# Optimization experiments

Measured on AMD Instinct MI355X. Metric: run time of the kernel, lower is better.

Reference implementation:

```python
import jax, jax.numpy as jnp
import numpy as np

NUM_NODES = 200000
NUM_EDGES = 500000
B = 4096            # batch size (src, dst, neg each B)
ND = 3 * B          # dst nodes of attention block
K = 10              # sampled neighbors per dst
N = ND * (1 + K)    # total tail nodes
D = 128             # dim_embed == dim_node
DE = 128            # dim_edge
DT = 128            # dim_time
H = 2               # num_heads
DIN = 2 * D + DE + DT  # GRUCell input dim


def time_encode(t, w, b):
    # tglite TimeEncode: cos(t * w + b)
    return jnp.cos(t[..., None] * w + b)


def gru_cell(x, h, w_ih, w_hh, b_ih, b_hh):
    # torch.nn.GRUCell, gate order [r, z, n]
    gi = x @ w_ih.T + b_ih
    gh = h @ w_hh.T + b_hh
    i_r, i_z, i_n = jnp.split(gi, 3, axis=-1)
    h_r, h_z, h_n = jnp.split(gh, 3, axis=-1)
    r = jax.nn.sigmoid(i_r + h_r)
    z = jax.nn.sigmoid(i_z + h_z)
    n = jnp.tanh(i_n + r * h_n)
    return (1.0 - z) * n + z * h


def setup_inputs() -> dict:
    key = jax.random.key(0)
    ks = jax.random.split(key, 40)
    p = lambda i, shape: jax.random.normal(ks[i], shape, dtype=jnp.float32) * 0.05
    return {
        "nodes": jax.random.randint(ks[0], (N,), 0, NUM_NODES),
        "eids": jax.random.randint(ks[1], (ND, K), 0, NUM_EDGES),
        "dt_nbr": jax.random.uniform(ks[2], (ND, K), dtype=jnp.float32) * 1000.0,
        "nfeat": p(3, (NUM_NODES, D)),
        "mem_data": p(4, (NUM_NODES, D)),
        "mem_time": jax.random.uniform(ks[5], (NUM_NODES,), dtype=jnp.float32) * 1000.0,
        "mail_data": p(6, (NUM_NODES, 2 * D + DE)),
        "mail_time": jax.random.uniform(ks[7], (NUM_NODES,), dtype=jnp.float32) * 1000.0,
        "efeat": p(8, (NUM_EDGES, DE)),
        "time_w": p(9, (DT,)),
        "time_b": p(10, (DT,)),
        "gru_w_ih": p(11, (3 * D, DIN)),
        "gru_w_hh": p(12, (3 * D, D)),
        "gru_b_ih": p(13, (3 * D,)),
        "gru_b_hh": p(14, (3 * D,)),
        "wq": p(15, (D, D + DT)), "bq": p(16, (D,)),
        "wk": p(17, (D, D + DE + DT)), "bk": p(18, (D,)),
        "wv": p(19, (D, D + DE + DT)), "bv": p(20, (D,)),
        "wo": p(21, (D, 2 * D)), "bo": p(22, (D,)),
        "ln_g": jnp.ones((D,), jnp.float32), "ln_b": jnp.zeros((D,), jnp.float32),
        "ep_sw": p(23, (D, D)), "ep_sb": p(24, (D,)),
        "ep_dw": p(25, (D, D)), "ep_db": p(26, (D,)),
        "ep_ow": p(27, (1, D)), "ep_ob": p(28, (1,)),
    }


def reference(nodes, eids, dt_nbr, nfeat, mem_data, mem_time, mail_data, mail_time,
              efeat, time_w, time_b, gru_w_ih, gru_w_hh, gru_b_ih, gru_b_hh,
              wq, bq, wk, bk, wv, bv, wo, bo, ln_g, ln_b,
              ep_sw, ep_sb, ep_dw, ep_db, ep_ow, ep_ob):
    # ---- update_memory: gather mailbox/memory, time-encode delta, GRUCell ----
    delta = mail_time[nodes] - mem_time[nodes]                  # [N]
    tenc = time_encode(delta, time_w, time_b)                   # [N, DT]
    mail = jnp.concatenate([mail_data[nodes], tenc], axis=1)    # [N, DIN]
    mem = gru_cell(mail, mem_data[nodes], gru_w_ih, gru_w_hh, gru_b_ih, gru_b_hh)  # [N, D]
    # (blk.g.mem.update(nodes, mem, mail_ts) is a persistent-state side effect)

    h = nfeat[nodes] + mem                                      # dst/src hidden states
    dst_h = h[:ND]                                              # [ND, D]
    src_h = h[ND:].reshape(ND, K, D)                            # [ND, K, D]

    # ---- TemporalAttnLayer (TGL-style multi-head attention over neighbors) ----
    zero_tenc = jnp.broadcast_to(jnp.cos(time_b), (ND, DT))     # time_encode(0)
    Q = jnp.concatenate([dst_h, zero_tenc], axis=1) @ wq.T + bq # [ND, D]
    tenc_n = time_encode(dt_nbr, time_w, time_b)                # [ND, K, DT]
    k_in = jnp.concatenate([src_h, efeat[eids], tenc_n], axis=-1)  # [ND, K, D+DE+DT]
    Kf = k_in @ wk.T + bk                                       # [ND, K, D]
    Vf = k_in @ wv.T + bv                                       # [ND, K, D]

    dh = D // H
    Qh = Q.reshape(ND, H, dh)
    Kh = Kf.reshape(ND, K, H, dh)
    Vh = Vf.reshape(ND, K, H, dh)
    att = jax.nn.softmax(jnp.einsum('nhd,nkhd->nkh', Qh, Kh), axis=1)  # [ND, K, H]
    agg = jnp.einsum('nkh,nkhd->nhd', att, Vh).reshape(ND, D)   # [ND, D]

    out = jnp.concatenate([dst_h, agg], axis=1) @ wo.T + bo     # [ND, D]
    out = jax.nn.relu(out)
    mu = out.mean(axis=-1, keepdims=True)
    var = out.var(axis=-1, keepdims=True)
    emb = ln_g * (out - mu) * jax.lax.rsqrt(var + 1e-5) + ln_b  # LayerNorm

    # ---- EdgePredictor over (src, dst) and (src, neg) splits ----
    src_e, dst_e, neg_e = emb[:B], emb[B:2 * B], emb[2 * B:]
    s_proj = src_e @ ep_sw.T + ep_sb
    pos = jax.nn.relu(s_proj + dst_e @ ep_dw.T + ep_db) @ ep_ow.T + ep_ob  # [B, 1]
    neg = jax.nn.relu(s_proj + neg_e @ ep_dw.T + ep_db) @ ep_ow.T + ep_ob  # [B, 1]
    return jnp.concatenate([pos, neg], axis=1)                  # [B, 2]
```

## Files before the change

### kernel.cpp

```cpp
#include <hip/hip_runtime.h>

constexpr int ND_   = 12288;
constexpr int K_    = 10;
constexpr int NTOT  = ND_ * (1 + K_);
constexpr int B_    = 4096;
constexpr int RKV   = ND_ * K_;

constexpr size_t OFF_QB   = 0;
constexpr size_t OFF_AGG  = 786432;
constexpr size_t OFF_HB   = 43253760;
constexpr size_t OFF_KVB  = 51904512;
constexpr size_t OFF_EMB  = 67633152;
constexpr size_t OFF_WCAT = 69206016;
constexpr size_t OFF_WKV  = 69369856;
constexpr size_t OFF_BCAT = 69419008;
constexpr size_t OFF_BKV  = 69419520;
constexpr size_t OFF_WQB  = 69419776;
constexpr size_t OFF_WOB  = 69427968;
constexpr size_t OFF_SWP  = 69444352;
constexpr size_t OFF_DWP  = 69460736;
constexpr size_t OFF_QZ   = 69477120;

#define DEVFN __device__ __forceinline__

typedef __attribute__((ext_vector_type(8))) short bf16x8;
typedef __attribute__((ext_vector_type(4))) float f32x4;
#define MFMA16(a, b, c) __builtin_amdgcn_mfma_f32_16x16x32_bf16((a), (b), (c), 0, 0, 0)

DEVFN unsigned short f2bf(float x) {
  unsigned int u = __float_as_uint(x);
  u = (u + 0x7FFFu + ((u >> 16) & 1u)) >> 16;
  return (unsigned short)u;
}
DEVFN float bf2f(unsigned short h) { return __uint_as_float(((unsigned int)h) << 16); }

DEVFN bf16x8 packcvt(float4 a, float4 b) {
  union { unsigned int u[4]; bf16x8 v; } r;
  asm("v_cvt_pk_bf16_f32 %0, %1, %2" : "=v"(r.u[0]) : "v"(a.x), "v"(a.y));
  asm("v_cvt_pk_bf16_f32 %0, %1, %2" : "=v"(r.u[1]) : "v"(a.z), "v"(a.w));
  asm("v_cvt_pk_bf16_f32 %0, %1, %2" : "=v"(r.u[2]) : "v"(b.x), "v"(b.y));
  asm("v_cvt_pk_bf16_f32 %0, %1, %2" : "=v"(r.u[3]) : "v"(b.z), "v"(b.w));
  return r.v;
}

DEVFN float dot4(const float4 a, const float4 b, float acc) {
  acc = fmaf(a.x, b.x, acc);
  acc = fmaf(a.y, b.y, acc);
  acc = fmaf(a.z, b.z, acc);
  acc = fmaf(a.w, b.w, acc);
  return acc;
}
DEVFN float fsig(float x)  { return __fdividef(1.0f, 1.0f + __expf(-x)); }
DEVFN float ftanh(float x) {
  x = fminf(fmaxf(x, -15.0f), 15.0f);
  const float t = __expf(2.0f * x);
  return __fdividef(t - 1.0f, t + 1.0f);
}

__global__ void k0_all(const float* __restrict__ w_ih, const float* __restrict__ w_hh,
                       const float* __restrict__ wk,   const float* __restrict__ wv,
                       const float* __restrict__ wq,   const float* __restrict__ wo,
                       const float* __restrict__ sw,   const float* __restrict__ dwm,
                       const float* __restrict__ b_ih, const float* __restrict__ b_hh,
                       const float* __restrict__ bk,   const float* __restrict__ bv,
                       const float* __restrict__ time_b, const float* __restrict__ bq,
                       unsigned short* __restrict__ WcatP, unsigned short* __restrict__ WkvP,
                       unsigned short* __restrict__ WqB,   unsigned short* __restrict__ WoB,
                       float4* __restrict__ SwP, float4* __restrict__ DwP,
                       float* __restrict__ bcat, float* __restrict__ bkv,
                       float* __restrict__ qzero)
{
  int gid = blockIdx.x * 256 + threadIdx.x;
  if (gid < 327680) {
    int f = gid >> 9, idx = gid & 511;
    int l = idx >> 3, j8 = idx & 7;
    int kt = f >> 5, nt = f & 31;
    int k = kt * 32 + (l >> 4) * 8 + j8;
    int c = nt * 16 + (l & 15);
    int q = c >> 7, jb = (c >> 6) & 1, g = (c >> 4) & 3, j = q * 32 + jb * 16 + (c & 15);
    float w;
    if (g == 0)      w = (k < 512) ? w_ih[(size_t)j * 512 + k]         : w_hh[(size_t)j * 128 + (k - 512)];
    else if (g == 1) w = (k < 512) ? w_ih[(size_t)(128 + j) * 512 + k] : w_hh[(size_t)(128 + j) * 128 + (k - 512)];
    else if (g == 2) w = (k < 512) ? w_ih[(size_t)(256 + j) * 512 + k] : 0.0f;
    else             w = (k < 512) ? 0.0f : w_hh[(size_t)(256 + j) * 128 + (k - 512)];
    WcatP[gid] = f2bf(w);
    return;
  }
  gid -= 327680;
  if (gid < 98304) {
    int f = gid >> 9, idx = gid & 511;
    int l = idx >> 3, j8 = idx & 7;
    int kt = f >> 4, nt = f & 15;
    int k = kt * 32 + (l >> 4) * 8 + j8;
    int c = nt * 16 + (l & 15);
    float w = (c < 128) ? wk[(size_t)c * 384 + k] : wv[(size_t)(c - 128) * 384 + k];
    WkvP[gid] = f2bf(w);
    return;
  }
  gid -= 98304;
  if (gid < 49152) {
    if (gid < 16384) {
      int f = gid >> 9, idx = gid & 511;
      int l = idx >> 3, j8 = idx & 7;
      int kt = f >> 3, nt = f & 7;
      int k = kt * 32 + (l >> 4) * 8 + j8;
      int c = nt * 16 + (l & 15);
      WqB[gid] = f2bf(wq[(size_t)c * 256 + k]);
    } else {
      int g2 = gid - 16384;
      int f = g2 >> 9, idx = g2 & 511;
      int l = idx >> 3, j8 = idx & 7;
      int kt = f >> 3, nt = f & 7;
      int k = kt * 32 + (l >> 4) * 8 + j8;
      int c = nt * 16 + (l & 15);
      WoB[g2] = f2bf(wo[(size_t)c * 256 + k]);
    }
    return;
  }
  gid -= 49152;
  if (gid < 8960) {
    if (gid < 4096) {
      int k4 = gid / 128, c = gid % 128;
      const float* s = sw + c * 128 + 4 * k4;
      SwP[gid] = make_float4(s[0], s[1], s[2], s[3]);
    } else if (gid < 8192) {
      int id = gid - 4096;
      int k4 = id / 128, c = id % 128;
      const float* s = dwm + c * 128 + 4 * k4;
      DwP[id] = make_float4(s[0], s[1], s[2], s[3]);
    } else if (gid < 8704) {
      int id = gid - 8192;
      int q = id >> 7, jb = (id >> 6) & 1, g = (id >> 4) & 3, lcc = id & 15;
      int j = q * 32 + jb * 16 + lcc;
      float b;
      if (g == 0)      b = b_ih[j] + b_hh[j];
      else if (g == 1) b = b_ih[128 + j] + b_hh[128 + j];
      else if (g == 2) b = b_ih[256 + j];
      else             b = b_hh[256 + j];
      bcat[id] = b;
    } else {
      int id = gid - 8704;
      bkv[id] = (id < 128) ? bk[id] : bv[id - 128];
    }
    return;
  }
  gid -= 8960;
  if (gid < 128) {
    float acc = bq[gid];
    for (int k = 0; k < 128; ++k)
      acc = fmaf(cosf(time_b[k]), wq[gid * 256 + 128 + k], acc);
    qzero[gid] = acc;
  }
}

__global__ __launch_bounds__(512, 4) void k1_fused(
    const int* __restrict__ nodes, const float* __restrict__ mail_data,
    const float* __restrict__ mem_data, const float* __restrict__ mail_time,
    const float* __restrict__ mem_time, const float* __restrict__ time_w,
    const float* __restrict__ time_b, const unsigned short* __restrict__ WcatP,
    const float* __restrict__ bcat, const float* __restrict__ nfeat,
    unsigned short* __restrict__ hb)
{
  __shared__ unsigned short As[20 * 1024];
  const int tid = threadIdx.x;
  const int rbase = blockIdx.x * 32;

  {
    const int sr = tid & 31, scol = tid >> 5;
    const int q = scol & 3, koff = scol >> 2;
    const int n = nodes[rbase + sr];
    const float drow = mail_time[n] - mem_time[n];
    const float* mailp = mail_data + (size_t)n * 384;
    const float* memp  = mem_data  + (size_t)n * 128;
    unsigned short* wb = As + (size_t)((sr >> 4) * 64 + q * 16 + (sr & 15)) * 8;
    #pragma unroll
    for (int i = 0; i < 5; ++i) {
      const int kt = 4 * i + koff;
      const int c0 = kt * 32 + q * 8;
      float4 v0, v1;
      if (c0 < 384) {
        v0 = *(const float4*)(mailp + c0);
        v1 = *(const float4*)(mailp + c0 + 4);
      } else if (c0 >= 512) {
        v0 = *(const float4*)(memp + c0 - 512);
        v1 = *(const float4*)(memp + c0 - 508);
      } else {
        const float4 w0 = *(const float4*)(time_w + c0 - 384);
        const float4 w1 = *(const float4*)(time_w + c0 - 380);
        const float4 b0 = *(const float4*)(time_b + c0 - 384);
        const float4 b1 = *(const float4*)(time_b + c0 - 380);
        v0.x = __cosf(fmaf(drow, w0.x, b0.x)); v0.y = __cosf(fmaf(drow, w0.y, b0.y));
        v0.z = __cosf(fmaf(drow, w0.z, b0.z)); v0.w = __cosf(fmaf(drow, w0.w, b0.w));
        v1.x = __cosf(fmaf(drow, w1.x, b1.x)); v1.y = __cosf(fmaf(drow, w1.y, b1.y));
        v1.z = __cosf(fmaf(drow, w1.z, b1.z)); v1.w = __cosf(fmaf(drow, w1.w, b1.w));
      }
      *(bf16x8*)(wb + (size_t)kt * 1024) = packcvt(v0, v1);
    }
  }
  __syncthreads();

  const int w = tid >> 6, l = tid & 63;
  const int lr = l >> 4, lc = l & 15;
  const unsigned short* Bp = WcatP + (size_t)(w * 4) * 512 + l * 8;
  const unsigned short* Ab = As + (size_t)l * 8;

  f32x4 acc[2][4];
  #pragma unroll
  for (int m = 0; m < 2; ++m)
    #pragma unroll
    for (int bn = 0; bn < 4; ++bn) acc[m][bn] = (f32x4){0.f, 0.f, 0.f, 0.f};

  #pragma unroll
  for (int kt = 0; kt < 20; ++kt) {
    const bf16x8 A0 = *(const bf16x8*)(Ab + (size_t)kt * 1024);
    const bf16x8 A1 = *(const bf16x8*)(Ab + (size_t)kt * 1024 + 512);
    #pragma unroll
    for (int bn = 0; bn < 4; ++bn) {
      const bf16x8 Bf = *(const bf16x8*)(Bp + ((size_t)kt * 32 + bn) * 512);
      acc[0][bn] = MFMA16(A0, Bf, acc[0][bn]);
      acc[1][bn] = MFMA16(A1, Bf, acc[1][bn]);
    }
  }

  const int jcol = (w >> 1) * 32 + (w & 1) * 16 + lc;
  float bg[4];
  #pragma unroll
  for (int g = 0; g < 4; ++g) bg[g] = bcat[w * 64 + g * 16 + lc];
  const int memkt = 16 + (w >> 1);
  const int qp = (w & 1) * 2 + (lc >> 3);
  const int el = lc & 7;

  #pragma unroll
  for (int mt = 0; mt < 2; ++mt) {
    #pragma unroll
    for (int rr = 0; rr < 4; ++rr) {
      const int rloc = mt * 16 + lr * 4 + rr;
      const int grow = rbase + rloc;
      const int n2   = nodes[grow];
      const float aR  = acc[mt][0][rr] + bg[0];
      const float aZ  = acc[mt][1][rr] + bg[1];
      const float aNi = acc[mt][2][rr] + bg[2];
      const float aNh = acc[mt][3][rr] + bg[3];
      const float r_  = fsig(aR);
      const float z_  = fsig(aZ);
      const float n_  = ftanh(aNi + r_ * aNh);
      const float mem = bf2f(As[(size_t)memkt * 1024 +
                                (size_t)(mt * 64 + qp * 16 + (rloc & 15)) * 8 + el]);
      const float h = nfeat[(size_t)n2 * 128 + jcol] + (1.0f - z_) * n_ + z_ * mem;
      hb[(size_t)grow * 128 + jcol] = f2bf(h);
    }
  }
}

DEVFN void k2s(const unsigned short* __restrict__ WkvP, int kt, int wn, int l,
               bf16x8 a, f32x4 (&acc)[4]) {
  #pragma unroll
  for (int bn = 0; bn < 4; ++bn) {
    const bf16x8 b = *(const bf16x8*)(WkvP + ((size_t)(kt * 16 + wn * 4 + bn) * 64 + l) * 8);
    acc[bn] = MFMA16(a, b, acc[bn]);
  }
}

__global__ __launch_bounds__(512) void k2_fused(
    const unsigned short* __restrict__ hb, const int* __restrict__ eids,
    const float* __restrict__ dt_nbr, const float* __restrict__ efeat,
    const float* __restrict__ time_w, const float* __restrict__ time_b,
    const unsigned short* __restrict__ WkvP, const float* __restrict__ bkv,
    unsigned short* __restrict__ KVb)
{
  const int w = threadIdx.x >> 6, l = threadIdx.x & 63;
  const int wm = w >> 2, wn = w & 3;
  const int lr = l >> 4, lc = l & 15;
  const int t16 = blockIdx.x * 2 + wm;
  const int rbase = t16 * 16;

  int eld = 0; float dld = 0.f;
  if (l < 16) { eld = eids[rbase + l]; dld = dt_nbr[rbase + l]; }
  const int   eid = __shfl(eld, lc);
  const float dt  = __shfl(dld, lc);

  const float* ep = efeat + (size_t)eid * 128 + lr * 8;
  bf16x8 ea[4];
  #pragma unroll
  for (int qq = 0; qq < 4; ++qq)
    ea[qq] = packcvt(((const float4*)(ep + qq * 32))[0], ((const float4*)(ep + qq * 32))[1]);
  const unsigned short* hp = hb + (size_t)(ND_ + rbase + lc) * 128 + lr * 8;
  bf16x8 hh[4];
  #pragma unroll
  for (int qq = 0; qq < 4; ++qq) hh[qq] = *(const bf16x8*)(hp + qq * 32);
  bf16x8 tt[4];
  #pragma unroll
  for (int qq = 0; qq < 4; ++qq) {
    const int c0 = qq * 32 + lr * 8;
    const float4 w0 = ((const float4*)(time_w + c0))[0];
    const float4 w1 = ((const float4*)(time_w + c0))[1];
    const float4 b0 = ((const float4*)(time_b + c0))[0];
    const float4 b1 = ((const float4*)(time_b + c0))[1];
    float4 u, v;
    u.x = __cosf(fmaf(dt, w0.x, b0.x)); u.y = __cosf(fmaf(dt, w0.y, b0.y));
    u.z = __cosf(fmaf(dt, w0.z, b0.z)); u.w = __cosf(fmaf(dt, w0.w, b0.w));
    v.x = __cosf(fmaf(dt, w1.x, b1.x)); v.y = __cosf(fmaf(dt, w1.y, b1.y));
    v.z = __cosf(fmaf(dt, w1.z, b1.z)); v.w = __cosf(fmaf(dt, w1.w, b1.w));
    tt[qq] = packcvt(u, v);
  }

  f32x4 acc[4];
  #pragma unroll
  for (int bn = 0; bn < 4; ++bn) acc[bn] = (f32x4){0.f, 0.f, 0.f, 0.f};

  #pragma unroll
  for (int qq = 0; qq < 4; ++qq) k2s(WkvP, qq, wn, l, hh[qq], acc);
  #pragma unroll
  for (int qq = 0; qq < 4; ++qq) k2s(WkvP, 4 + qq, wn, l, ea[qq], acc);
  #pragma unroll
  for (int qq = 0; qq < 4; ++qq) k2s(WkvP, 8 + qq, wn, l, tt[qq], acc);

  float bb[4];
  #pragma unroll
  for (int bn = 0; bn < 4; ++bn) bb[bn] = bkv[wn * 64 + bn * 16 + lc];

  #pragma unroll
  for (int rr = 0; rr < 4; ++rr) {
    const size_t grow = (size_t)(rbase + lr * 4 + rr);
    #pragma unroll
    for (int bn = 0; bn < 4; ++bn)
      KVb[grow * 256 + wn * 64 + bn * 16 + lc] = f2bf(acc[bn][rr] + bb[bn]);
  }
}

__global__ __launch_bounds__(512) void kQ_gemm(
    const unsigned short* __restrict__ hb, const unsigned short* __restrict__ WqB,
    const float* __restrict__ qzero, unsigned short* __restrict__ Qb)
{
  const int w = threadIdx.x >> 6, l = threadIdx.x & 63;
  const int wm = w >> 2, wn = w & 3;
  const int lr = l >> 4, lc = l & 15;
  const int t16base = blockIdx.x * 4 + wm * 2;
  const unsigned short* Ar0 = hb + (size_t)(t16base * 16 + lc) * 128 + lr * 8;
  const unsigned short* Ar1 = Ar0 + 16 * 128;

  f32x4 acc[2][2];
  #pragma unroll
  for (int m = 0; m < 2; ++m)
    #pragma unroll
    for (int bn = 0; bn < 2; ++bn) acc[m][bn] = (f32x4){0.f, 0.f, 0.f, 0.f};

  #pragma unroll
  for (int kt = 0; kt < 4; ++kt) {
    const bf16x8 a0 = *(const bf16x8*)(Ar0 + kt * 32);
    const bf16x8 a1 = *(const bf16x8*)(Ar1 + kt * 32);
    #pragma unroll
    for (int bn = 0; bn < 2; ++bn) {
      const bf16x8 b = *(const bf16x8*)(WqB + ((size_t)(kt * 8 + wn * 2 + bn) * 64 + l) * 8);
      acc[0][bn] = MFMA16(a0, b, acc[0][bn]);
      acc[1][bn] = MFMA16(a1, b, acc[1][bn]);
    }
  }

  #pragma unroll
  for (int mt = 0; mt < 2; ++mt)
    #pragma unroll
    for (int rr = 0; rr < 4; ++rr) {
      const int row = (t16base + mt) * 16 + lr * 4 + rr;
      #pragma unroll
      for (int bn = 0; bn < 2; ++bn) {
        const int col = (wn * 2 + bn) * 16 + lc;
        Qb[(size_t)row * 128 + col] = f2bf(acc[mt][bn][rr] + qzero[col]);
      }
    }
}

__global__ __launch_bounds__(256) void kAtt(
    const unsigned short* __restrict__ Qb, const unsigned short* __restrict__ KVb,
    unsigned short* __restrict__ aggb)
{
  const int w = threadIdx.x >> 6, l = threadIdx.x & 63;
  const int i = blockIdx.x * 4 + w;
  const float q0 = bf2f(Qb[(size_t)i * 128 + l]);
  const float q1 = bf2f(Qb[(size_t)i * 128 + 64 + l]);
  const unsigned short* base = KVb + (size_t)i * K_ * 256;

  float s0[K_], s1[K_], v0[K_], v1[K_];
  #pragma unroll
  for (int kk = 0; kk < K_; ++kk) {
    const unsigned short* rp = base + kk * 256;
    const float k0 = bf2f(rp[l]);
    const float k1 = bf2f(rp[64 + l]);
    v0[kk] = bf2f(rp[128 + l]);
    v1[kk] = bf2f(rp[192 + l]);
    float p0 = q0 * k0, p1 = q1 * k1;
    #pragma unroll
    for (int t = 32; t; t >>= 1) { p0 += __shfl_xor(p0, t); p1 += __shfl_xor(p1, t); }
    s0[kk] = p0; s1[kk] = p1;
  }
  float m0 = s0[0], m1 = s1[0];
  #pragma unroll
  for (int kk = 1; kk < K_; ++kk) { m0 = fmaxf(m0, s0[kk]); m1 = fmaxf(m1, s1[kk]); }
  float sum0 = 0.f, sum1 = 0.f, a0 = 0.f, a1 = 0.f;
  #pragma unroll
  for (int kk = 0; kk < K_; ++kk) {
    const float e0 = __expf(s0[kk] - m0);
    const float e1 = __expf(s1[kk] - m1);
    sum0 += e0; sum1 += e1;
    a0 += e0 * v0[kk]; a1 += e1 * v1[kk];
  }
  aggb[(size_t)i * 128 + l]      = f2bf(__fdividef(a0, sum0));
  aggb[(size_t)i * 128 + 64 + l] = f2bf(__fdividef(a1, sum1));
}

__global__ __launch_bounds__(512) void kO_ln(
    const unsigned short* __restrict__ hb, const unsigned short* __restrict__ aggb,
    const unsigned short* __restrict__ WoB, const float* __restrict__ bo,
    const float* __restrict__ ln_g, const float* __restrict__ ln_b,
    float* __restrict__ emb)
{
  __shared__ float ps[64][4], pq[64][4];
  const int w = threadIdx.x >> 6, l = threadIdx.x & 63;
  const int wm = w >> 2, wn = w & 3;
  const int lr = l >> 4, lc = l & 15;
  const int t16base = blockIdx.x * 4 + wm * 2;
  const unsigned short* Ah0 = hb   + (size_t)(t16base * 16 + lc) * 128 + lr * 8;
  const unsigned short* Ah1 = Ah0 + 16 * 128;
  const unsigned short* Ag0 = aggb + (size_t)(t16base * 16 + lc) * 128 + lr * 8;
  const unsigned short* Ag1 = Ag0 + 16 * 128;

  f32x4 acc[2][2];
  #pragma unroll
  for (int m = 0; m < 2; ++m)
    #pragma unroll
    for (int bn = 0; bn < 2; ++bn) acc[m][bn] = (f32x4){0.f, 0.f, 0.f, 0.f};

  #pragma unroll
  for (int kt = 0; kt < 8; ++kt) {
    const bf16x8 a0 = (kt < 4) ? *(const bf16x8*)(Ah0 + kt * 32)
                               : *(const bf16x8*)(Ag0 + (kt - 4) * 32);
    const bf16x8 a1 = (kt < 4) ? *(const bf16x8*)(Ah1 + kt * 32)
                               : *(const bf16x8*)(Ag1 + (kt - 4) * 32);
    #pragma unroll
    for (int bn = 0; bn < 2; ++bn) {
      const bf16x8 b = *(const bf16x8*)(WoB + ((size_t)(kt * 8 + wn * 2 + bn) * 64 + l) * 8);
      acc[0][bn] = MFMA16(a0, b, acc[0][bn]);
      acc[1][bn] = MFMA16(a1, b, acc[1][bn]);
    }
  }

  const int c0 = (wn * 2) * 16 + lc, c1 = c0 + 16;
  const float b0v = bo[c0], b1v = bo[c1];
  float xv0[2][4], xv1[2][4];
  #pragma unroll
  for (int mt = 0; mt < 2; ++mt)
    #pragma unroll
    for (int rr = 0; rr < 4; ++rr) {
      const float x0 = fmaxf(acc[mt][0][rr] + b0v, 0.f);
      const float x1 = fmaxf(acc[mt][1][rr] + b1v, 0.f);
      xv0[mt][rr] = x0; xv1[mt][rr] = x1;
      float s = x0 + x1, q = x0 * x0 + x1 * x1;
      #pragma unroll
      for (int t = 8; t; t >>= 1) { s += __shfl_xor(s, t); q += __shfl_xor(q, t); }
      const int rloc = (wm * 2 + mt) * 16 + lr * 4 + rr;
      if (lc == 0) { ps[rloc][wn] = s; pq[rloc][wn] = q; }
    }
  __syncthreads();
  const float g0 = ln_g[c0], g1 = ln_g[c1], lb0 = ln_b[c0], lb1 = ln_b[c1];
  #pragma unroll
  for (int mt = 0; mt < 2; ++mt)
    #pragma unroll
    for (int rr = 0; rr < 4; ++rr) {
      const int rloc = (wm * 2 + mt) * 16 + lr * 4 + rr;
      const int row  = blockIdx.x * 64 + rloc;
      const float sum = ps[rloc][0] + ps[rloc][1] + ps[rloc][2] + ps[rloc][3];
      const float sq  = pq[rloc][0] + pq[rloc][1] + pq[rloc][2] + pq[rloc][3];
      const float mu  = sum * (1.0f / 128.0f);
      const float var = sq * (1.0f / 128.0f) - mu * mu;
      const float rs  = rsqrtf(var + 1e-5f);
      emb[(size_t)row * 128 + c0] = g0 * (xv0[mt][rr] - mu) * rs + lb0;
      emb[(size_t)row * 128 + c1] = g1 * (xv1[mt][rr] - mu) * rs + lb1;
    }
}

__global__ __launch_bounds__(128) void k3_ep(
    const float* __restrict__ emb, const float4* __restrict__ SwP,
    const float4* __restrict__ DwP, const float* __restrict__ ep_sb,
    const float* __restrict__ ep_db, const float* __restrict__ ep_ow,
    const float* __restrict__ ep_ob, float* __restrict__ out)
{
  __shared__ float se[128], de[128], ne[128];
  __shared__ float redp[2], redn[2];
  const int c = threadIdx.x;
  const int i = blockIdx.x;
  se[c] = emb[(size_t)i * 128 + c];
  de[c] = emb[(size_t)(B_ + i) * 128 + c];
  ne[c] = emb[(size_t)(2 * B_ + i) * 128 + c];
  __syncthreads();
  float sacc = ep_sb[c], dacc = ep_db[c], nacc = ep_db[c];
  for (int k4 = 0; k4 < 32; ++k4) {
    const float4 sw = SwP[k4 * 128 + c];
    const float4 dw = DwP[k4 * 128 + c];
    sacc = dot4(((const float4*)se)[k4], sw, sacc);
    dacc = dot4(((const float4*)de)[k4], dw, dacc);
    nacc = dot4(((const float4*)ne)[k4], dw, nacc);
  }
  const float ow = ep_ow[c];
  float pp = fmaxf(sacc + dacc, 0.f) * ow;
  float pn = fmaxf(sacc + nacc, 0.f) * ow;
  for (int t = 32; t; t >>= 1) { pp += __shfl_xor(pp, t); pn += __shfl_xor(pn, t); }
  if ((c & 63) == 0) { redp[c >> 6] = pp; redn[c >> 6] = pn; }
  __syncthreads();
  if (c == 0) {
    const float ob = ep_ob[0];
    out[i * 2]     = redp[0] + redp[1] + ob;
    out[i * 2 + 1] = redn[0] + redn[1] + ob;
  }
}

extern "C" void kernel_launch(void* const* d_in, const int* in_sizes, int n_in,
                              void* d_out, int out_size, void* d_ws, size_t ws_size,
                              hipStream_t stream) {
  const int*   nodes     = (const int*)d_in[0];
  const int*   eids      = (const int*)d_in[1];
  const float* dt_nbr    = (const float*)d_in[2];
  const float* nfeat     = (const float*)d_in[3];
  const float* mem_data  = (const float*)d_in[4];
  const float* mem_time  = (const float*)d_in[5];
  const float* mail_data = (const float*)d_in[6];
  const float* mail_time = (const float*)d_in[7];
  const float* efeat     = (const float*)d_in[8];
  const float* time_w    = (const float*)d_in[9];
  const float* time_b    = (const float*)d_in[10];
  const float* gru_w_ih  = (const float*)d_in[11];
  const float* gru_w_hh  = (const float*)d_in[12];
  const float* gru_b_ih  = (const float*)d_in[13];
  const float* gru_b_hh  = (const float*)d_in[14];
  const float* wq        = (const float*)d_in[15];
  const float* bq        = (const float*)d_in[16];
  const float* wk        = (const float*)d_in[17];
  const float* bk        = (const float*)d_in[18];
  const float* wv        = (const float*)d_in[19];
  const float* bv        = (const float*)d_in[20];
  const float* wo        = (const float*)d_in[21];
  const float* bo        = (const float*)d_in[22];
  const float* ln_g      = (const float*)d_in[23];
  const float* ln_b      = (const float*)d_in[24];
  const float* ep_sw     = (const float*)d_in[25];
  const float* ep_sb     = (const float*)d_in[26];
  const float* ep_dw     = (const float*)d_in[27];
  const float* ep_db     = (const float*)d_in[28];
  const float* ep_ow     = (const float*)d_in[29];
  const float* ep_ob     = (const float*)d_in[30];
  float* out = (float*)d_out;
  float* ws  = (float*)d_ws;

  unsigned short* Qb    = (unsigned short*)(ws + OFF_QB);
  unsigned short* aggb  = (unsigned short*)(ws + OFF_AGG);
  unsigned short* hb    = (unsigned short*)(ws + OFF_HB);
  unsigned short* KVb   = (unsigned short*)(ws + OFF_KVB);
  float*          emb   = ws + OFF_EMB;
  unsigned short* WcatP = (unsigned short*)(ws + OFF_WCAT);
  unsigned short* WkvP  = (unsigned short*)(ws + OFF_WKV);
  float*          bcat  = ws + OFF_BCAT;
  float*          bkv   = ws + OFF_BKV;
  unsigned short* WqB   = (unsigned short*)(ws + OFF_WQB);
  unsigned short* WoB   = (unsigned short*)(ws + OFF_WOB);
  float4*         SwP   = (float4*)(ws + OFF_SWP);
  float4*         DwP   = (float4*)(ws + OFF_DWP);
  float*          qzero = ws + OFF_QZ;

  k0_all<<<1892, 256, 0, stream>>>(gru_w_ih, gru_w_hh, wk, wv, wq, wo, ep_sw, ep_dw,
                                   gru_b_ih, gru_b_hh, bk, bv, time_b, bq,
                                   WcatP, WkvP, WqB, WoB, SwP, DwP, bcat, bkv, qzero);
  k1_fused<<<NTOT / 32, 512, 0, stream>>>(nodes, mail_data, mem_data, mail_time,
                                          mem_time, time_w, time_b, WcatP, bcat,
                                          nfeat, hb);
  k2_fused<<<RKV / 32, 512, 0, stream>>>(hb, eids, dt_nbr, efeat, time_w, time_b,
                                         WkvP, bkv, KVb);
  kQ_gemm<<<ND_ / 64, 512, 0, stream>>>(hb, WqB, qzero, Qb);
  kAtt<<<ND_ / 4, 256, 0, stream>>>(Qb, KVb, aggb);
  kO_ln<<<ND_ / 64, 512, 0, stream>>>(hb, aggb, WoB, bo, ln_g, ln_b, emb);
  k3_ep<<<B_, 128, 0, stream>>>(emb, SwP, DwP, ep_sb, ep_db, ep_ow, ep_ob, out);
}
```

Before: 407.3 us.

## Double-buffer k1 A-tile gather in LDS to overlap loads with MFMA

The GRU k1 kernel used to stage all 20 K-tiles of the gathered input (mail, time encoding, memory) in a 40KB LDS buffer before any MFMA work. It now keeps two 4-tile chunks, gathering the next chunk into registers while the MFMAs consume the current one, then writing it to the other buffer and syncing. This shrinks LDS from 40KB to 16KB and raises the launch-bounds occupancy hint from 4 to 8 blocks, aiming to hide gather latency. The cost is extra barriers and register pressure. The final chunk lands in buffer 0, so the memory-state read in the epilogue still finds its data.

```diff
diff --git a/kernel.cpp b/kernel.cpp
--- a/kernel.cpp
+++ b/kernel.cpp
@@ -153,7 +153,7 @@
   }
 }
 
-__global__ __launch_bounds__(512, 4) void k1_fused(
+__global__ __launch_bounds__(512, 8) void k1_fused(
     const int* __restrict__ nodes, const float* __restrict__ mail_data,
     const float* __restrict__ mem_data, const float* __restrict__ mail_time,
     const float* __restrict__ mem_time, const float* __restrict__ time_w,
@@ -161,48 +161,51 @@
     const float* __restrict__ bcat, const float* __restrict__ nfeat,
     unsigned short* __restrict__ hb)
 {
-  __shared__ unsigned short As[20 * 1024];
+  __shared__ unsigned short As[2][4 * 1024];
   const int tid = threadIdx.x;
   const int rbase = blockIdx.x * 32;
 
+  const int ktl  = tid >> 7;
+  const int slot = tid & 127;
+  const int shalf = slot >> 6, sq = (slot >> 4) & 3, sr15 = slot & 15;
+  const int srow = shalf * 16 + sr15;
+  const int sn = nodes[rbase + srow];
+  const float sdrow = mail_time[sn] - mem_time[sn];
+  const float* mailp = mail_data + (size_t)sn * 384;
+  const float* memp  = mem_data  + (size_t)sn * 128;
+  unsigned short* const wslot0 = &As[0][(size_t)ktl * 1024 + (size_t)slot * 8];
+  unsigned short* const wslot1 = &As[1][(size_t)ktl * 1024 + (size_t)slot * 8];
+
+  auto gather = [&](int kt, float4& v0, float4& v1) {
+    const int c0 = kt * 32 + sq * 8;
+    if (c0 < 384) {
+      v0 = *(const float4*)(mailp + c0);
+      v1 = *(const float4*)(mailp + c0 + 4);
+    } else if (c0 >= 512) {
+      v0 = *(const float4*)(memp + c0 - 512);
+      v1 = *(const float4*)(memp + c0 - 508);
+    } else {
+      const float4 w0 = *(const float4*)(time_w + c0 - 384);
+      const float4 w1 = *(const float4*)(time_w + c0 - 380);
+      const float4 b0 = *(const float4*)(time_b + c0 - 384);
+      const float4 b1 = *(const float4*)(time_b + c0 - 380);
+      v0.x = __cosf(fmaf(sdrow, w0.x, b0.x)); v0.y = __cosf(fmaf(sdrow, w0.y, b0.y));
+      v0.z = __cosf(fmaf(sdrow, w0.z, b0.z)); v0.w = __cosf(fmaf(sdrow, w0.w, b0.w));
+      v1.x = __cosf(fmaf(sdrow, w1.x, b1.x)); v1.y = __cosf(fmaf(sdrow, w1.y, b1.y));
+      v1.z = __cosf(fmaf(sdrow, w1.z, b1.z)); v1.w = __cosf(fmaf(sdrow, w1.w, b1.w));
+    }
+  };
+
   {
-    const int sr = tid & 31, scol = tid >> 5;
-    const int q = scol & 3, koff = scol >> 2;
-    const int n = nodes[rbase + sr];
-    const float drow = mail_time[n] - mem_time[n];
-    const float* mailp = mail_data + (size_t)n * 384;
-    const float* memp  = mem_data  + (size_t)n * 128;
-    unsigned short* wb = As + (size_t)((sr >> 4) * 64 + q * 16 + (sr & 15)) * 8;
-    #pragma unroll
-    for (int i = 0; i < 5; ++i) {
-      const int kt = 4 * i + koff;
-      const int c0 = kt * 32 + q * 8;
-      float4 v0, v1;
-      if (c0 < 384) {
-        v0 = *(const float4*)(mailp + c0);
-        v1 = *(const float4*)(mailp + c0 + 4);
-      } else if (c0 >= 512) {
-        v0 = *(const float4*)(memp + c0 - 512);
-        v1 = *(const float4*)(memp + c0 - 508);
-      } else {
-        const float4 w0 = *(const float4*)(time_w + c0 - 384);
-        const float4 w1 = *(const float4*)(time_w + c0 - 380);
-        const float4 b0 = *(const float4*)(time_b + c0 - 384);
-        const float4 b1 = *(const float4*)(time_b + c0 - 380);
-        v0.x = __cosf(fmaf(drow, w0.x, b0.x)); v0.y = __cosf(fmaf(drow, w0.y, b0.y));
-        v0.z = __cosf(fmaf(drow, w0.z, b0.z)); v0.w = __cosf(fmaf(drow, w0.w, b0.w));
-        v1.x = __cosf(fmaf(drow, w1.x, b1.x)); v1.y = __cosf(fmaf(drow, w1.y, b1.y));
-        v1.z = __cosf(fmaf(drow, w1.z, b1.z)); v1.w = __cosf(fmaf(drow, w1.w, b1.w));
-      }
-      *(bf16x8*)(wb + (size_t)kt * 1024) = packcvt(v0, v1);
-    }
+    float4 v0, v1;
+    gather(ktl, v0, v1);
+    *(bf16x8*)wslot0 = packcvt(v0, v1);
   }
   __syncthreads();
 
   const int w = tid >> 6, l = tid & 63;
   const int lr = l >> 4, lc = l & 15;
   const unsigned short* Bp = WcatP + (size_t)(w * 4) * 512 + l * 8;
-  const unsigned short* Ab = As + (size_t)l * 8;
 
   f32x4 acc[2][4];
   #pragma unroll
@@ -211,14 +214,25 @@
     for (int bn = 0; bn < 4; ++bn) acc[m][bn] = (f32x4){0.f, 0.f, 0.f, 0.f};
 
   #pragma unroll
-  for (int kt = 0; kt < 20; ++kt) {
-    const bf16x8 A0 = *(const bf16x8*)(Ab + (size_t)kt * 1024);
-    const bf16x8 A1 = *(const bf16x8*)(Ab + (size_t)kt * 1024 + 512);
-    #pragma unroll
-    for (int bn = 0; bn < 4; ++bn) {
-      const bf16x8 Bf = *(const bf16x8*)(Bp + ((size_t)kt * 32 + bn) * 512);
-      acc[0][bn] = MFMA16(A0, Bf, acc[0][bn]);
-      acc[1][bn] = MFMA16(A1, Bf, acc[1][bn]);
+  for (int c = 0; c < 5; ++c) {
+    float4 nv0, nv1;
+    if (c < 4) gather((c + 1) * 4 + ktl, nv0, nv1);
+    const unsigned short* Ab = &As[c & 1][(size_t)l * 8];
+    #pragma unroll
+    for (int k4 = 0; k4 < 4; ++k4) {
+      const int kt = c * 4 + k4;
+      const bf16x8 A0 = *(const bf16x8*)(Ab + (size_t)k4 * 1024);
+      const bf16x8 A1 = *(const bf16x8*)(Ab + (size_t)k4 * 1024 + 512);
+      #pragma unroll
+      for (int bn = 0; bn < 4; ++bn) {
+        const bf16x8 Bf = *(const bf16x8*)(Bp + ((size_t)kt * 32 + bn) * 512);
+        acc[0][bn] = MFMA16(A0, Bf, acc[0][bn]);
+        acc[1][bn] = MFMA16(A1, Bf, acc[1][bn]);
+      }
+    }
+    if (c < 4) {
+      *(bf16x8*)((c & 1) ? wslot0 : wslot1) = packcvt(nv0, nv1);
+      __syncthreads();
     }
   }
 
@@ -226,7 +240,7 @@
   float bg[4];
   #pragma unroll
   for (int g = 0; g < 4; ++g) bg[g] = bcat[w * 64 + g * 16 + lc];
-  const int memkt = 16 + (w >> 1);
+  const int memktl = w >> 1;
   const int qp = (w & 1) * 2 + (lc >> 3);
   const int el = lc & 7;
 
@@ -244,8 +258,8 @@
       const float r_  = fsig(aR);
       const float z_  = fsig(aZ);
       const float n_  = ftanh(aNi + r_ * aNh);
-      const float mem = bf2f(As[(size_t)memkt * 1024 +
-                                (size_t)(mt * 64 + qp * 16 + (rloc & 15)) * 8 + el]);
+      const float mem = bf2f(As[0][(size_t)memktl * 1024 +
+                                   (size_t)(mt * 64 + qp * 16 + (rloc & 15)) * 8 + el]);
       const float h = nfeat[(size_t)n2 * 128 + jcol] + (1.0f - z_) * n_ + z_ * mem;
       hb[(size_t)grow * 128 + jcol] = f2bf(h);
     }
```

Measured after the change: 517.9 us. +27.2%, slower.

## Double-buffer GRU input staging in k1 and overlap gathers with MFMA

Applied to the files above, without the earlier changes.

Replaces the single 20-k-tile shared staging buffer in the fused GRU kernel with a two-slot buffer of 4 k-tiles each. Each 128-column chunk is gathered into registers while the previous chunk feeds the MFMA loop. Rows are stored with a rotating swizzle to spread LDS bank accesses, and the nfeat row is loaded coalesced into shared memory instead of being scattered per output element. This cuts LDS footprint and hides gather latency, at the cost of extra barriers per chunk.

```diff
diff --git a/kernel.cpp b/kernel.cpp
--- a/kernel.cpp
+++ b/kernel.cpp
@@ -161,48 +161,55 @@
     const float* __restrict__ bcat, const float* __restrict__ nfeat,
     unsigned short* __restrict__ hb)
 {
-  __shared__ unsigned short As[20 * 1024];
+  __shared__ unsigned short As[2][4 * 1024];
+  __shared__ float nf[32][132];
   const int tid = threadIdx.x;
   const int rbase = blockIdx.x * 32;
 
+  const int r = tid >> 4, j = tid & 15;
+  const int half = r >> 4, r15 = r & 15;
+  const int n = nodes[rbase + r];
+  const float drow = mail_time[n] - mem_time[n];
+  const float* mailp = mail_data + (size_t)n * 384;
+  const float* memp  = mem_data  + (size_t)n * 128;
+
+  const int ktg0 = j >> 2, q = j & 3;
+
+  auto gather = [&](int c, float4& v0, float4& v1) {
+    if (c < 3) {
+      const float* s = mailp + c * 128 + j * 8;
+      v0 = *(const float4*)s; v1 = *(const float4*)(s + 4);
+    } else if (c == 4) {
+      const float* s = memp + j * 8;
+      v0 = *(const float4*)s; v1 = *(const float4*)(s + 4);
+    } else {
+      const float4 w0 = *(const float4*)(time_w + j * 8);
+      const float4 w1 = *(const float4*)(time_w + j * 8 + 4);
+      const float4 b0 = *(const float4*)(time_b + j * 8);
+      const float4 b1 = *(const float4*)(time_b + j * 8 + 4);
+      v0.x = __cosf(fmaf(drow, w0.x, b0.x)); v0.y = __cosf(fmaf(drow, w0.y, b0.y));
+      v0.z = __cosf(fmaf(drow, w0.z, b0.z)); v0.w = __cosf(fmaf(drow, w0.w, b0.w));
+      v1.x = __cosf(fmaf(drow, w1.x, b1.x)); v1.y = __cosf(fmaf(drow, w1.y, b1.y));
+      v1.z = __cosf(fmaf(drow, w1.z, b1.z)); v1.w = __cosf(fmaf(drow, w1.w, b1.w));
+    }
+  };
+  auto wstage = [&](int b, int c, float4 v0, float4 v1) {
+    const int kt = c * 4 + ktg0;
+    const int rowp = (r15 + kt) & 15;
+    unsigned short* wb = &As[b][(size_t)ktg0 * 1024 + (size_t)(half * 64 + q * 16 + rowp) * 8];
+    *(bf16x8*)wb = packcvt(v0, v1);
+  };
+
   {
-    const int sr = tid & 31, scol = tid >> 5;
-    const int q = scol & 3, koff = scol >> 2;
-    const int n = nodes[rbase + sr];
-    const float drow = mail_time[n] - mem_time[n];
-    const float* mailp = mail_data + (size_t)n * 384;
-    const float* memp  = mem_data  + (size_t)n * 128;
-    unsigned short* wb = As + (size_t)((sr >> 4) * 64 + q * 16 + (sr & 15)) * 8;
-    #pragma unroll
-    for (int i = 0; i < 5; ++i) {
-      const int kt = 4 * i + koff;
-      const int c0 = kt * 32 + q * 8;
-      float4 v0, v1;
-      if (c0 < 384) {
-        v0 = *(const float4*)(mailp + c0);
-        v1 = *(const float4*)(mailp + c0 + 4);
-      } else if (c0 >= 512) {
-        v0 = *(const float4*)(memp + c0 - 512);
-        v1 = *(const float4*)(memp + c0 - 508);
-      } else {
-        const float4 w0 = *(const float4*)(time_w + c0 - 384);
-        const float4 w1 = *(const float4*)(time_w + c0 - 380);
-        const float4 b0 = *(const float4*)(time_b + c0 - 384);
-        const float4 b1 = *(const float4*)(time_b + c0 - 380);
-        v0.x = __cosf(fmaf(drow, w0.x, b0.x)); v0.y = __cosf(fmaf(drow, w0.y, b0.y));
-        v0.z = __cosf(fmaf(drow, w0.z, b0.z)); v0.w = __cosf(fmaf(drow, w0.w, b0.w));
-        v1.x = __cosf(fmaf(drow, w1.x, b1.x)); v1.y = __cosf(fmaf(drow, w1.y, b1.y));
-        v1.z = __cosf(fmaf(drow, w1.z, b1.z)); v1.w = __cosf(fmaf(drow, w1.w, b1.w));
-      }
-      *(bf16x8*)(wb + (size_t)kt * 1024) = packcvt(v0, v1);
-    }
+    float4 v0, v1;
+    gather(0, v0, v1);
+    wstage(0, 0, v0, v1);
   }
   __syncthreads();
 
   const int w = tid >> 6, l = tid & 63;
   const int lr = l >> 4, lc = l & 15;
   const unsigned short* Bp = WcatP + (size_t)(w * 4) * 512 + l * 8;
-  const unsigned short* Ab = As + (size_t)l * 8;
 
   f32x4 acc[2][4];
   #pragma unroll
@@ -210,23 +217,44 @@
     #pragma unroll
     for (int bn = 0; bn < 4; ++bn) acc[m][bn] = (f32x4){0.f, 0.f, 0.f, 0.f};
 
-  #pragma unroll
-  for (int kt = 0; kt < 20; ++kt) {
-    const bf16x8 A0 = *(const bf16x8*)(Ab + (size_t)kt * 1024);
-    const bf16x8 A1 = *(const bf16x8*)(Ab + (size_t)kt * 1024 + 512);
-    #pragma unroll
-    for (int bn = 0; bn < 4; ++bn) {
-      const bf16x8 Bf = *(const bf16x8*)(Bp + ((size_t)kt * 32 + bn) * 512);
-      acc[0][bn] = MFMA16(A0, Bf, acc[0][bn]);
-      acc[1][bn] = MFMA16(A1, Bf, acc[1][bn]);
-    }
-  }
+  float4 nfv0, nfv1;
+  #pragma unroll
+  for (int c = 0; c < 5; ++c) {
+    float4 nv0, nv1;
+    if (c < 4) gather(c + 1, nv0, nv1);
+    else {
+      const float* np = nfeat + (size_t)n * 128 + j * 8;
+      nfv0 = *(const float4*)np; nfv1 = *(const float4*)(np + 4);
+    }
+    #pragma unroll
+    for (int ktl = 0; ktl < 4; ++ktl) {
+      const int kt = c * 4 + ktl;
+      const int rowp = (lc + kt) & 15;
+      const unsigned short* Ab = &As[c & 1][(size_t)ktl * 1024 + (size_t)(lr * 16 + rowp) * 8];
+      const bf16x8 A0 = *(const bf16x8*)Ab;
+      const bf16x8 A1 = *(const bf16x8*)(Ab + 512);
+      #pragma unroll
+      for (int bn = 0; bn < 4; ++bn) {
+        const bf16x8 Bf = *(const bf16x8*)(Bp + ((size_t)kt * 32 + bn) * 512);
+        acc[0][bn] = MFMA16(A0, Bf, acc[0][bn]);
+        acc[1][bn] = MFMA16(A1, Bf, acc[1][bn]);
+      }
+    }
+    if (c < 4) {
+      wstage((c + 1) & 1, c + 1, nv0, nv1);
+      __syncthreads();
+    }
+  }
+
+  *(float4*)(&nf[r][j * 8])     = nfv0;
+  *(float4*)(&nf[r][j * 8 + 4]) = nfv1;
+  __syncthreads();
 
   const int jcol = (w >> 1) * 32 + (w & 1) * 16 + lc;
   float bg[4];
   #pragma unroll
   for (int g = 0; g < 4; ++g) bg[g] = bcat[w * 64 + g * 16 + lc];
-  const int memkt = 16 + (w >> 1);
+  const int memktl = w >> 1;
   const int qp = (w & 1) * 2 + (lc >> 3);
   const int el = lc & 7;
 
@@ -236,7 +264,7 @@
     for (int rr = 0; rr < 4; ++rr) {
       const int rloc = mt * 16 + lr * 4 + rr;
       const int grow = rbase + rloc;
-      const int n2   = nodes[grow];
+      const int rowp = ((rloc & 15) + 16 + memktl) & 15;
       const float aR  = acc[mt][0][rr] + bg[0];
       const float aZ  = acc[mt][1][rr] + bg[1];
       const float aNi = acc[mt][2][rr] + bg[2];
@@ -244,9 +272,9 @@
       const float r_  = fsig(aR);
       const float z_  = fsig(aZ);
       const float n_  = ftanh(aNi + r_ * aNh);
-      const float mem = bf2f(As[(size_t)memkt * 1024 +
-                                (size_t)(mt * 64 + qp * 16 + (rloc & 15)) * 8 + el]);
-      const float h = nfeat[(size_t)n2 * 128 + jcol] + (1.0f - z_) * n_ + z_ * mem;
+      const float mem = bf2f(As[0][(size_t)memktl * 1024 +
+                                   (size_t)(mt * 64 + qp * 16 + rowp) * 8 + el]);
+      const float h = nf[rloc][jcol] + (1.0f - z_) * n_ + z_ * mem;
       hb[(size_t)grow * 128 + jcol] = f2bf(h);
     }
   }
```

New measurement: 378.4 us, median of 2. 7.1% less time.
